# Optimization experiments

Hardware: AMD Instinct MI355X
Metric: run time of the kernel (lower is better)

The kernel has to match this reference:

```python
import jax, jax.numpy as jnp
import numpy as np

NCLASSES = 100
ALPHA = 1.0
CLIP = False


def setup_inputs() -> dict:
    key = jax.random.key(0)
    k1, k2, k3 = jax.random.split(key, 3)
    N, D, C = 8192, 10000, NCLASSES
    encoded = jax.random.normal(k1, (N, D), dtype=jnp.float32)
    class_hvs = jax.random.normal(k2, (C, D), dtype=jnp.float32)
    targets = jax.random.randint(k3, (N,), 0, C, dtype=jnp.int64)
    return {"encoded": encoded, "class_hvs": class_hvs, "targets": targets}


def reference(encoded, class_hvs, targets):
    # Cosine-similarity scores: [N, C]
    scores = jnp.matmul(encoded, class_hvs.T)
    norm_enc = jnp.linalg.norm(encoded, axis=1)        # [N]
    norm_cls = jnp.linalg.norm(class_hvs, axis=1)      # [C]
    scores = scores / (norm_enc[:, None] * norm_cls[None, :])

    # Training-path perceptron update (torch code runs this under no_grad)
    preds = jnp.argmax(scores, axis=1)                 # [N]
    wrong = (targets != preds).astype(encoded.dtype)   # [N]
    enc_wrong = encoded * wrong[:, None]               # masked rows, zeros elsewhere

    # sum of misclassified encodings grouped by true label / predicted label
    add_t = jax.ops.segment_sum(enc_wrong, targets, num_segments=NCLASSES) * ALPHA
    sub_p = jax.ops.segment_sum(enc_wrong, preds, num_segments=NCLASSES)
    if CLIP:
        add_t = jnp.clip(add_t, -1.0, 1.0)
        sub_p = jnp.clip(sub_p, -1.0, 1.0)
    new_class_hvs = class_hvs + add_t * ALPHA - sub_p * ALPHA
    new_class_hvs = jax.lax.stop_gradient(new_class_hvs)

    return scores, new_class_hvs
```

## Files before the change

### kernel.cpp

```cpp
#include <hip/hip_runtime.h>
#include <hip/hip_bf16.h>
#include <math.h>

#define NROWS 8192
#define DDIM  10000
#define NCLS  100

#define KSPLIT 8
#define KS64   157
#define BM 128
#define UPD_DC 64
#define DPAD 10048

#define SCORES_N (NROWS*NCLS)
#define NCHUNK8 1256
#define BP_CHUNKS (NCHUNK8*128)
#define PREPB_BLOCKS ((BP_CHUNKS + 255) / 256)

#define WS_NORMCLS 0
#define WS_NRM     128
#define WS_SCP     (WS_NRM + KSPLIT*NROWS)
#define WS_TP      (WS_SCP + KSPLIT*SCORES_N)
#define WS_BPH     (WS_TP + NROWS + 128)
#define WS_BPL     (WS_BPH + BP_CHUNKS*4)
#define WS_PART    (WS_BPL + BP_CHUNKS*4)

typedef _Float16 f16;
typedef f16 f16x8 __attribute__((ext_vector_type(8)));
typedef float f32x4 __attribute__((ext_vector_type(4)));

#define SBAR()  __builtin_amdgcn_s_barrier()
#define SCHED() __builtin_amdgcn_sched_barrier(0)

__global__ __launch_bounds__(256) void prep(const float* __restrict__ cls,
                                            float* __restrict__ ws)
{
    int bx = blockIdx.x;
    if (bx < NCLS) {
        int c = bx;
        const float* row = cls + (size_t)c * DDIM;
        float s = 0.f;
        for (int d = threadIdx.x; d < DDIM; d += 256) {
            float v = row[d];
            s = fmaf(v, v, s);
        }
        #pragma unroll
        for (int off = 32; off; off >>= 1) s += __shfl_xor(s, off, 64);
        __shared__ float red[4];
        int w = threadIdx.x >> 6, l = threadIdx.x & 63;
        if (l == 0) red[w] = s;
        __syncthreads();
        if (threadIdx.x == 0) {
            float t = red[0] + red[1] + red[2] + red[3];
            ws[WS_NORMCLS + c] = sqrtf(t);
        }
    } else {
        int c = (bx - NCLS) * 256 + threadIdx.x;
        if (c >= BP_CHUNKS) return;
        int col = c & 127, k8 = c >> 7;
        f16x8 hi, lo;
        #pragma unroll
        for (int j = 0; j < 8; ++j) {
            int k = k8 * 8 + j;
            float v = (col < NCLS && k < DDIM) ? cls[(size_t)col * DDIM + k] : 0.f;
            f16 h = (f16)v;
            hi[j] = h;
            lo[j] = (f16)(v - (float)h);
        }
        ((f16x8*)(ws + WS_BPH))[c] = hi;
        ((f16x8*)(ws + WS_BPL))[c] = lo;
    }
}

__global__ __launch_bounds__(256, 2) void gemm_mfma(const float* __restrict__ enc,
                                                    float* __restrict__ ws)
{
    __shared__ f16 Bh[2][8*128*8], Bl[2][8*128*8];

    int tid = threadIdx.x;
    int w = __builtin_amdgcn_readfirstlane(tid >> 6);
    int l = tid & 63;
    int lane15 = l & 15, lg = l >> 4;
    int r0 = blockIdx.x * BM;
    int ky = blockIdx.y;
    int s_beg = (KS64 * ky) / KSPLIT;
    int s_end = (KS64 * (ky + 1)) / KSPLIT;

    const float* aptr0 = enc + (size_t)(r0 + w * 32 + lane15) * DDIM;
    const float* aptr1 = aptr0 + (size_t)16 * DDIM;
    const f16* bph = (const f16*)(ws + WS_BPH);
    const f16* bpl = (const f16*)(ws + WS_BPL);

    f32x4 acc[2][7] = {};
    float nsq0 = 0.f, nsq1 = 0.f;

    float4 ar[8];
    f16x8 bsh[2][2], bsl[2][2];

    #define LOAD_A(S) do {                                               \
        int kA_ = (S) * 64 + lg * 8;                                     \
        int kB_ = kA_ + 32;                                              \
        int a0_ = (kA_ + 4 <= DDIM) ? kA_ : 0;                           \
        int a1_ = (kA_ + 8 <= DDIM) ? (kA_ + 4) : 0;                     \
        int b0_ = (kB_ + 4 <= DDIM) ? kB_ : 0;                           \
        int b1_ = (kB_ + 8 <= DDIM) ? (kB_ + 4) : 0;                     \
        ar[0] = *(const float4*)(aptr0 + a0_);                           \
        ar[1] = *(const float4*)(aptr0 + a1_);                           \
        ar[2] = *(const float4*)(aptr0 + b0_);                           \
        ar[3] = *(const float4*)(aptr0 + b1_);                           \
        ar[4] = *(const float4*)(aptr1 + a0_);                           \
        ar[5] = *(const float4*)(aptr1 + a1_);                           \
        ar[6] = *(const float4*)(aptr1 + b0_);                           \
        ar[7] = *(const float4*)(aptr1 + b1_);                           \
    } while (0)

    #define LOAD_B(S) do {                                               \
        _Pragma("unroll")                                                \
        for (int j_ = 0; j_ < 2; ++j_) {                                 \
            size_t base_ = ((size_t)((S) * 8 + 2 * w + j_) * 128) * 8;   \
            bsh[j_][0] = *(const f16x8*)(bph + base_ + (size_t)l * 8);   \
            bsh[j_][1] = *(const f16x8*)(bph + base_ + (size_t)(l + 64) * 8); \
            bsl[j_][0] = *(const f16x8*)(bpl + base_ + (size_t)l * 8);   \
            bsl[j_][1] = *(const f16x8*)(bpl + base_ + (size_t)(l + 64) * 8); \
        }                                                                \
    } while (0)

    LOAD_A(s_beg);
    LOAD_B(s_beg);

    for (int S = s_beg; S < s_end; ++S) {
        int cur = S & 1;

        f16x8 ah[2][2], al[2][2];
        #pragma unroll
        for (int r = 0; r < 2; ++r) {
            float& nsq = r ? nsq1 : nsq0;
            #pragma unroll
            for (int ks = 0; ks < 2; ++ks) {
                float4 p0 = ar[r * 4 + ks * 2], p1 = ar[r * 4 + ks * 2 + 1];
                float v[8] = {p0.x, p0.y, p0.z, p0.w, p1.x, p1.y, p1.z, p1.w};
                int kb = S * 64 + ks * 32 + lg * 8;
                if (kb + 8 > DDIM) {
                    #pragma unroll
                    for (int j = 0; j < 8; ++j) if (kb + j >= DDIM) v[j] = 0.f;
                }
                #pragma unroll
                for (int j = 0; j < 8; ++j) {
                    f16 h = (f16)v[j];
                    ah[r][ks][j] = h;
                    al[r][ks][j] = (f16)(v[j] - (float)h);
                    nsq = fmaf(v[j], v[j], nsq);
                }
            }
        }

        #pragma unroll
        for (int j = 0; j < 2; ++j) {
            int kg = 2 * w + j;
            int s0 = kg * 128 + (l ^ kg);
            int s1 = kg * 128 + ((l + 64) ^ kg);
            *(f16x8*)&Bh[cur][s0 * 8] = bsh[j][0];
            *(f16x8*)&Bh[cur][s1 * 8] = bsh[j][1];
            *(f16x8*)&Bl[cur][s0 * 8] = bsl[j][0];
            *(f16x8*)&Bl[cur][s1 * 8] = bsl[j][1];
        }

        {
            int Sn = (S + 1 < s_end) ? (S + 1) : S;
            LOAD_A(Sn);
            LOAD_B(Sn);
        }

        SCHED();
        asm volatile("s_waitcnt lgkmcnt(0)" ::: "memory");
        SBAR();
        SCHED();

        #pragma unroll
        for (int ks = 0; ks < 2; ++ks) {
            int kg = ks * 4 + lg;
            #pragma unroll
            for (int nt = 0; nt < 7; ++nt) {
                int colS = (nt * 16 + lane15) ^ kg;
                f16x8 bh = *(const f16x8*)&Bh[cur][(kg * 128 + colS) * 8];
                f16x8 bl = *(const f16x8*)&Bl[cur][(kg * 128 + colS) * 8];
                acc[0][nt] = __builtin_amdgcn_mfma_f32_16x16x32_f16(ah[0][ks], bh, acc[0][nt], 0, 0, 0);
                acc[0][nt] = __builtin_amdgcn_mfma_f32_16x16x32_f16(al[0][ks], bh, acc[0][nt], 0, 0, 0);
                acc[0][nt] = __builtin_amdgcn_mfma_f32_16x16x32_f16(ah[0][ks], bl, acc[0][nt], 0, 0, 0);
                acc[1][nt] = __builtin_amdgcn_mfma_f32_16x16x32_f16(ah[1][ks], bh, acc[1][nt], 0, 0, 0);
                acc[1][nt] = __builtin_amdgcn_mfma_f32_16x16x32_f16(al[1][ks], bh, acc[1][nt], 0, 0, 0);
                acc[1][nt] = __builtin_amdgcn_mfma_f32_16x16x32_f16(ah[1][ks], bl, acc[1][nt], 0, 0, 0);
            }
        }
    }

    float* scp = ws + WS_SCP + (size_t)ky * SCORES_N;
    #pragma unroll
    for (int mt = 0; mt < 2; ++mt) {
        #pragma unroll
        for (int nt = 0; nt < 7; ++nt) {
            int gcol = nt * 16 + lane15;
            if (gcol < NCLS) {
                #pragma unroll
                for (int j = 0; j < 4; ++j) {
                    int grow = r0 + w * 32 + mt * 16 + lg * 4 + j;
                    scp[(size_t)grow * NCLS + gcol] = acc[mt][nt][j];
                }
            }
        }
    }

    nsq0 += __shfl_xor(nsq0, 16, 64);
    nsq0 += __shfl_xor(nsq0, 32, 64);
    nsq1 += __shfl_xor(nsq1, 16, 64);
    nsq1 += __shfl_xor(nsq1, 32, 64);
    if (l < 16) {
        ws[WS_NRM + (size_t)ky * NROWS + r0 + w * 32 + l] = nsq0;
        ws[WS_NRM + (size_t)ky * NROWS + r0 + w * 32 + 16 + l] = nsq1;
    }
}

__global__ __launch_bounds__(256) void finalize(const int* __restrict__ targets,
                                                float* __restrict__ out,
                                                float* __restrict__ ws)
{
    int w = threadIdx.x >> 6, l = threadIdx.x & 63;
    int row = blockIdx.x * 4 + w;
    const float* scp = ws + WS_SCP;

    float n2 = 0.f;
    #pragma unroll
    for (int ky = 0; ky < KSPLIT; ++ky) n2 += ws[WS_NRM + (size_t)ky * NROWS + row];
    float ne = sqrtf(n2);

    float best; int bi;
    {
        int c = l;
        float dsum = 0.f;
        #pragma unroll
        for (int ky = 0; ky < KSPLIT; ++ky)
            dsum += scp[(size_t)ky * SCORES_N + (size_t)row * NCLS + c];
        float s = dsum / (ne * ws[WS_NORMCLS + c]);
        out[(size_t)row * NCLS + c] = s;
        best = s; bi = c;
    }
    if (l + 64 < NCLS) {
        int c = l + 64;
        float dsum = 0.f;
        #pragma unroll
        for (int ky = 0; ky < KSPLIT; ++ky)
            dsum += scp[(size_t)ky * SCORES_N + (size_t)row * NCLS + c];
        float s = dsum / (ne * ws[WS_NORMCLS + c]);
        out[(size_t)row * NCLS + c] = s;
        if (s > best) { best = s; bi = c; }
    }
    #pragma unroll
    for (int off = 32; off; off >>= 1) {
        float ov = __shfl_xor(best, off, 64);
        int   oi = __shfl_xor(bi, off, 64);
        if (ov > best || (ov == best && oi < bi)) { best = ov; bi = oi; }
    }
    if (l == 0) {
        int tgt = targets[row];
        ((int*)ws)[WS_TP + row] = (tgt != bi) ? ((tgt << 8) | bi) : -1;
    }
}

__global__ __launch_bounds__(128) void update_scatter(const float* __restrict__ enc,
                                                      float* __restrict__ ws)
{
    __shared__ float acc[2][102][UPD_DC];
    int tid = threadIdx.x;
    int wv = tid >> 6, l = tid & 63;

    for (int i = tid; i < 2 * 102 * UPD_DC; i += 128) (&acc[0][0][0])[i] = 0.f;
    __syncthreads();

    int d = blockIdx.x * UPD_DC + l;
    int dc = (d < DDIM) ? d : (DDIM - 1);
    const int* tp = ((const int*)ws) + WS_TP;
    int r0 = blockIdx.y * 2048 + wv * 1024;

    for (int it = 0; it < 1024; it += 16) {
        float v[16]; int tv[16];
        #pragma unroll
        for (int u = 0; u < 16; ++u) {
            int r = r0 + it + u;
            v[u]  = enc[(size_t)r * DDIM + dc];
            tv[u] = tp[r];
        }
        #pragma unroll
        for (int u = 0; u < 16; ++u) {
            int t = (tv[u] >= 0) ? (tv[u] >> 8)  : 100;
            int p = (tv[u] >= 0) ? (tv[u] & 255) : 101;
            acc[wv][t][l] += v[u];
            acc[wv][p][l] -= v[u];
        }
    }
    __syncthreads();

    float* part = ws + WS_PART + (size_t)blockIdx.y * NCLS * DPAD;
    for (int idx = tid; idx < NCLS * UPD_DC; idx += 128) {
        int c = idx >> 6, dl = idx & 63;
        int dd = blockIdx.x * UPD_DC + dl;
        if (dd < DDIM)
            part[(size_t)c * DPAD + dd] = acc[0][c][dl] + acc[1][c][dl];
    }
}

__global__ __launch_bounds__(256) void update_reduce(const float* __restrict__ cls,
                                                     float* __restrict__ out,
                                                     const float* __restrict__ ws)
{
    int idx = blockIdx.x * 256 + threadIdx.x;
    if (idx >= NCLS * DDIM) return;
    int c = idx / DDIM, d = idx - c * DDIM;
    const float* part = ws + WS_PART;
    size_t o = (size_t)c * DPAD + d;
    float s = part[o] + part[(size_t)1 * NCLS * DPAD + o]
            + part[(size_t)2 * NCLS * DPAD + o] + part[(size_t)3 * NCLS * DPAD + o];
    out[SCORES_N + (size_t)c * DDIM + d] = cls[(size_t)c * DDIM + d] + s;
}

extern "C" void kernel_launch(void* const* d_in, const int* in_sizes, int n_in,
                              void* d_out, int out_size, void* d_ws, size_t ws_size,
                              hipStream_t stream)
{
    const float* enc = (const float*)d_in[0];
    const float* cls = (const float*)d_in[1];
    const int*   tgt = (const int*)d_in[2];
    float* out = (float*)d_out;
    float* ws  = (float*)d_ws;

    prep<<<NCLS + PREPB_BLOCKS, 256, 0, stream>>>(cls, ws);

    dim3 g1(NROWS / BM, KSPLIT);
    gemm_mfma<<<g1, 256, 0, stream>>>(enc, ws);

    finalize<<<NROWS / 4, 256, 0, stream>>>(tgt, out, ws);

    dim3 g3((DDIM + UPD_DC - 1) / UPD_DC, 4);
    update_scatter<<<g3, 128, 0, stream>>>(enc, ws);

    update_reduce<<<(NCLS * DDIM + 255) / 256, 256, 0, stream>>>(cls, out, ws);
}
```

Before: 246.7 us.

## Replace LDS scatter class update with one-hot MFMA matmul and reorder GEMM grid

The per-class segment sums of misclassified rows, previously done by scattering into shared-memory accumulators, are now computed as a matrix multiply. A signed one-hot (target minus prediction) matrix is multiplied by the encoded rows on f16 MFMA, software-prefetching the next row slice, and the row split grows from 4 to 8 partial buffers. The GEMM grid is also transposed so K-split blocks for the same row tile launch adjacently. This removes LDS read-modify-write traffic in exchange for rounding the encoded values to f16 and doubling the partial-sum write and reduce traffic.

```diff
diff --git a/kernel.cpp b/kernel.cpp
--- a/kernel.cpp
+++ b/kernel.cpp
@@ -9,7 +9,7 @@
 #define KSPLIT 8
 #define KS64   157
 #define BM 128
-#define UPD_DC 64
+#define UPD_NY 8
 #define DPAD 10048
 
 #define SCORES_N (NROWS*NCLS)
@@ -81,8 +81,8 @@
     int w = __builtin_amdgcn_readfirstlane(tid >> 6);
     int l = tid & 63;
     int lane15 = l & 15, lg = l >> 4;
-    int r0 = blockIdx.x * BM;
-    int ky = blockIdx.y;
+    int ky = blockIdx.x;
+    int r0 = blockIdx.y * BM;
     int s_beg = (KS64 * ky) / KSPLIT;
     int s_end = (KS64 * (ky + 1)) / KSPLIT;
 
@@ -266,45 +266,75 @@
     }
 }
 
-__global__ __launch_bounds__(128) void update_scatter(const float* __restrict__ enc,
-                                                      float* __restrict__ ws)
-{
-    __shared__ float acc[2][102][UPD_DC];
+__global__ __launch_bounds__(256) void update_mfma(const float* __restrict__ enc,
+                                                   float* __restrict__ ws)
+{
     int tid = threadIdx.x;
-    int wv = tid >> 6, l = tid & 63;
-
-    for (int i = tid; i < 2 * 102 * UPD_DC; i += 128) (&acc[0][0][0])[i] = 0.f;
-    __syncthreads();
-
-    int d = blockIdx.x * UPD_DC + l;
+    int w = tid >> 6, l = tid & 63;
+    int lane15 = l & 15, lg = l >> 4;
+    int dbase = blockIdx.x * 64 + w * 16;
+    int d = dbase + lane15;
     int dc = (d < DDIM) ? d : (DDIM - 1);
+    int rbase = blockIdx.y * (NROWS / UPD_NY);
     const int* tp = ((const int*)ws) + WS_TP;
-    int r0 = blockIdx.y * 2048 + wv * 1024;
-
-    for (int it = 0; it < 1024; it += 16) {
-        float v[16]; int tv[16];
-        #pragma unroll
-        for (int u = 0; u < 16; ++u) {
-            int r = r0 + it + u;
-            v[u]  = enc[(size_t)r * DDIM + dc];
-            tv[u] = tp[r];
-        }
-        #pragma unroll
-        for (int u = 0; u < 16; ++u) {
-            int t = (tv[u] >= 0) ? (tv[u] >> 8)  : 100;
-            int p = (tv[u] >= 0) ? (tv[u] & 255) : 101;
-            acc[wv][t][l] += v[u];
-            acc[wv][p][l] -= v[u];
-        }
-    }
-    __syncthreads();
+    const float* ep = enc + dc;
+
+    f32x4 acc[7] = {};
+
+    float bw[8]; int tv[8];
+    #define UM_ISSUE(KS) do {                                           \
+        int r0_ = rbase + (KS) * 32 + lg * 8;                           \
+        _Pragma("unroll")                                               \
+        for (int j_ = 0; j_ < 8; ++j_) {                                \
+            bw[j_] = ep[(size_t)(r0_ + j_) * DDIM];                     \
+            tv[j_] = tp[r0_ + j_];                                      \
+        }                                                               \
+    } while (0)
+
+    UM_ISSUE(0);
+    for (int ks = 0; ks < 32; ++ks) {
+        float bc[8]; int tc[8];
+        #pragma unroll
+        for (int j = 0; j < 8; ++j) { bc[j] = bw[j]; tc[j] = tv[j]; }
+        {
+            int kn = (ks + 1 < 32) ? (ks + 1) : 31;
+            UM_ISSUE(kn);
+        }
+
+        f16x8 bfrag;
+        #pragma unroll
+        for (int j = 0; j < 8; ++j) bfrag[j] = (f16)bc[j];
+
+        int tt[8], pp[8];
+        #pragma unroll
+        for (int j = 0; j < 8; ++j) {
+            tt[j] = (tc[j] >= 0) ? (tc[j] >> 8)  : 102;
+            pp[j] = (tc[j] >= 0) ? (tc[j] & 255) : 102;
+        }
+
+        #pragma unroll
+        for (int ct = 0; ct < 7; ++ct) {
+            int c = ct * 16 + lane15;
+            f16x8 afrag;
+            #pragma unroll
+            for (int j = 0; j < 8; ++j) {
+                afrag[j] = (f16)((tt[j] == c) ? 1.f : 0.f) - (f16)((pp[j] == c) ? 1.f : 0.f);
+            }
+            acc[ct] = __builtin_amdgcn_mfma_f32_16x16x32_f16(afrag, bfrag, acc[ct], 0, 0, 0);
+        }
+    }
 
     float* part = ws + WS_PART + (size_t)blockIdx.y * NCLS * DPAD;
-    for (int idx = tid; idx < NCLS * UPD_DC; idx += 128) {
-        int c = idx >> 6, dl = idx & 63;
-        int dd = blockIdx.x * UPD_DC + dl;
-        if (dd < DDIM)
-            part[(size_t)c * DPAD + dd] = acc[0][c][dl] + acc[1][c][dl];
+    if (d < DDIM) {
+        #pragma unroll
+        for (int ct = 0; ct < 7; ++ct) {
+            #pragma unroll
+            for (int j = 0; j < 4; ++j) {
+                int c = ct * 16 + lg * 4 + j;
+                if (c < NCLS)
+                    part[(size_t)c * DPAD + d] = acc[ct][j];
+            }
+        }
     }
 }
 
@@ -317,8 +347,10 @@
     int c = idx / DDIM, d = idx - c * DDIM;
     const float* part = ws + WS_PART;
     size_t o = (size_t)c * DPAD + d;
-    float s = part[o] + part[(size_t)1 * NCLS * DPAD + o]
-            + part[(size_t)2 * NCLS * DPAD + o] + part[(size_t)3 * NCLS * DPAD + o];
+    float s = 0.f;
+    #pragma unroll
+    for (int ry = 0; ry < UPD_NY; ++ry)
+        s += part[(size_t)ry * NCLS * DPAD + o];
     out[SCORES_N + (size_t)c * DDIM + d] = cls[(size_t)c * DDIM + d] + s;
 }
 
@@ -334,13 +366,13 @@
 
     prep<<<NCLS + PREPB_BLOCKS, 256, 0, stream>>>(cls, ws);
 
-    dim3 g1(NROWS / BM, KSPLIT);
+    dim3 g1(KSPLIT, NROWS / BM);
     gemm_mfma<<<g1, 256, 0, stream>>>(enc, ws);
 
     finalize<<<NROWS / 4, 256, 0, stream>>>(tgt, out, ws);
 
-    dim3 g3((DDIM + UPD_DC - 1) / UPD_DC, 4);
-    update_scatter<<<g3, 128, 0, stream>>>(enc, ws);
+    dim3 g3((DDIM + 63) / 64, UPD_NY);
+    update_mfma<<<g3, 256, 0, stream>>>(enc, ws);
 
     update_reduce<<<(NCLS * DDIM + 255) / 256, 256, 0, stream>>>(cls, out, ws);
 }
```

New measurement: 241.1 us. 2.3% less time.
